# Performance work log

Measured on AMD Instinct MI355X. Metric: run time of the kernel, lower is better.

The kernel has to match this reference:

```python
import jax, jax.numpy as jnp
import numpy as np
import math

R, C, B, E = 64, 256, 1, 768
H, DK, F = 8, 96, 3072
EPS = 1e-5


def _ln(x, w, b):
    m = jnp.mean(x, axis=-1, keepdims=True)
    v = jnp.var(x, axis=-1, keepdims=True)
    return (x - m) / jnp.sqrt(v + EPS) * w + b


def _lin(x, w, b):
    # torch Linear: y = x @ W^T + b, W: [out, in]
    return jnp.einsum('...i,oi->...o', x, w) + b


def setup_inputs() -> dict:
    key = jax.random.key(0)
    ks = jax.random.split(key, 16)
    w = lambda k, s: jax.random.normal(k, s, dtype=jnp.float32) * 0.02
    z = lambda s: jnp.zeros(s, dtype=jnp.float32)
    o = lambda s: jnp.ones(s, dtype=jnp.float32)
    return {
        'x': jax.random.normal(ks[0], (R, C, B, E), dtype=jnp.float32),
        'ln_row_w': o((E,)), 'ln_row_b': z((E,)),
        'row_q_w': w(ks[1], (E, E)), 'row_q_b': z((E,)),
        'row_k_w': w(ks[2], (E, E)), 'row_k_b': z((E,)),
        'row_v_w': w(ks[3], (E, E)), 'row_v_b': z((E,)),
        'row_o_w': w(ks[4], (E, E)), 'row_o_b': z((E,)),
        'ln_col_w': o((E,)), 'ln_col_b': z((E,)),
        'col_q_w': w(ks[5], (E, E)), 'col_q_b': z((E,)),
        'col_k_w': w(ks[6], (E, E)), 'col_k_b': z((E,)),
        'col_v_w': w(ks[7], (E, E)), 'col_v_b': z((E,)),
        'col_o_w': w(ks[8], (E, E)), 'col_o_b': z((E,)),
        'ln_ffn_w': o((E,)), 'ln_ffn_b': z((E,)),
        'fc1_w': w(ks[9], (F, E)), 'fc1_b': z((F,)),
        'fc2_w': w(ks[10], (E, F)), 'fc2_b': z((E,)),
    }


def reference(x, ln_row_w, ln_row_b, row_q_w, row_q_b, row_k_w, row_k_b,
              row_v_w, row_v_b, row_o_w, row_o_b,
              ln_col_w, ln_col_b, col_q_w, col_q_b, col_k_w, col_k_b,
              col_v_w, col_v_b, col_o_w, col_o_b,
              ln_ffn_w, ln_ffn_b, fc1_w, fc1_b, fc2_w, fc2_b):
    r, c, n, e = x.shape  # n_rows, n_cols, batch, embed

    # ---- Row self-attention (pre-LN residual block) ----
    xn = _ln(x, ln_row_w, ln_row_b)
    scaling = (DK ** -0.5) / math.sqrt(r)  # align_scaling: extra 1/sqrt(n_rows)
    q = _lin(xn, row_q_w, row_q_b).reshape(r, c, n, H, DK) * scaling
    k = _lin(xn, row_k_w, row_k_b).reshape(r, c, n, H, DK)
    v = _lin(xn, row_v_w, row_v_b).reshape(r, c, n, H, DK)
    row_logits = jnp.einsum('rinhd,rjnhd->hnij', q, k)  # sums over rows
    row_probs = jax.nn.softmax(row_logits, axis=-1)     # [H, B, C, C]
    rc = jnp.einsum('hnij,rjnhd->rinhd', row_probs, v).reshape(r, c, n, e)
    x = x + _lin(rc, row_o_w, row_o_b)

    # ---- Column self-attention (pre-LN residual block) ----
    xn = _ln(x, ln_col_w, ln_col_b)
    q = _lin(xn, col_q_w, col_q_b).reshape(r, c, n, H, DK) * (DK ** -0.5)
    k = _lin(xn, col_k_w, col_k_b).reshape(r, c, n, H, DK)
    v = _lin(xn, col_v_w, col_v_b).reshape(r, c, n, H, DK)
    col_logits = jnp.einsum('icnhd,jcnhd->hcnij', q, k)
    col_probs = jax.nn.softmax(col_logits, axis=-1)     # [H, C, B, R, R]
    cc = jnp.einsum('hcnij,jcnhd->icnhd', col_probs, v).reshape(r, c, n, e)
    x = x + _lin(cc, col_o_w, col_o_b)

    # ---- Feed-forward (pre-LN residual block) ----
    xn = _ln(x, ln_ffn_w, ln_ffn_b)
    h = jax.nn.gelu(_lin(xn, fc1_w, fc1_b), approximate=False)
    x = x + _lin(h, fc2_w, fc2_b)

    return x, row_probs, col_probs
```

## Files before the change

kernel.cpp:

```cpp
#include <hip/hip_runtime.h>
#include <cstdint>

typedef unsigned short u16;
typedef __attribute__((ext_vector_type(8))) short short8;
typedef __attribute__((ext_vector_type(4))) short short4v;
typedef __attribute__((ext_vector_type(4))) float floatx4;

#define DEV __device__ __forceinline__

DEV float bf2f(u16 u) { union { uint32_t i; float f; } w; w.i = ((uint32_t)u) << 16; return w.f; }
DEV u16 f2bf(float f) {
  union { float f; uint32_t i; } w; w.f = f;
  uint32_t x = w.i;
  return (u16)((x + 0x7fffu + ((x >> 16) & 1u)) >> 16);
}

DEV float fast_gelu(float x) {
  const float y = x * 0.70710678118f;
  const float ay = fabsf(y);
  const float t = 1.f / (1.f + 0.3275911f * ay);
  const float poly = t * (0.254829592f + t * (-0.284496736f +
                     t * (1.421413741f + t * (-1.453152027f + t * 1.061405429f))));
  const float er = 1.f - poly * __expf(-y * y);
  const float erf_y = __builtin_copysignf(er, y);
  return 0.5f * x * (1.f + erf_y);
}

DEV void async_copy16(const u16* g, u16* l) {
  __builtin_amdgcn_global_load_lds(
      (const __attribute__((address_space(1))) void*)(uintptr_t)g,
      (__attribute__((address_space(3))) void*)(uint32_t)(uintptr_t)l,
      16, 0, 0);
}

struct CvtArgs {
  const float* src[10];
  float scale[10];
};
__global__ __launch_bounds__(256) void cvt_all(CvtArgs a, u16* __restrict__ dst) {
  const size_t e = ((size_t)blockIdx.x * 256 + threadIdx.x) * 4;
  if (e >= 9437184) return;
  int reg, N, K;
  size_t base;
  if (e < 4718592) { reg = (int)(e / 589824); base = (size_t)reg * 589824; N = 768; K = 768; }
  else if (e < 7077888) { reg = 8; base = 4718592; N = 3072; K = 768; }
  else { reg = 9; base = 7077888; N = 768; K = 3072; }
  const int NKT = K >> 5;
  const size_t r = e - base;
  const int tile = (int)(r >> 12);
  const int nt = tile / NKT, kt = tile - nt * NKT;
  const int rem = (int)(r & 4095);
  const int c = rem >> 10, row = (rem >> 3) & 127, j = rem & 7;
  const int n = nt * 128 + row, k = kt * 32 + c * 8 + j;
  const float sc = a.scale[reg];
  floatx4 f = *(const floatx4*)(a.src[reg] + (size_t)n * K + k);
  short4v o;
#pragma unroll
  for (int q = 0; q < 4; ++q) o[q] = (short)f2bf(f[q] * sc);
  *(short4v*)(dst + e) = o;
}

__global__ __launch_bounds__(256) void bias_pack(const float* __restrict__ qb,
                                                 const float* __restrict__ kb,
                                                 const float* __restrict__ vb,
                                                 float sq, float* __restrict__ out) {
  const int i = blockIdx.x * 256 + threadIdx.x;
  if (i >= 2304) return;
  const int buf = i / 768, c = i - buf * 768;
  out[i] = buf == 0 ? qb[c] * sq : (buf == 1 ? kb[c] : vb[c]);
}

template<bool INF32>
__global__ __launch_bounds__(256) void ln_kernel(const void* __restrict__ in,
                                                 const float* __restrict__ w,
                                                 const float* __restrict__ b,
                                                 u16* __restrict__ out) {
  const int wid = threadIdx.x >> 6, lane = threadIdx.x & 63;
  const int row = blockIdx.x * 4 + wid;
  const size_t base = (size_t)row * 768;
  float v[12];
#pragma unroll
  for (int p = 0; p < 3; ++p) {
    const int e = p * 256 + lane * 4;
    if constexpr (INF32) {
      floatx4 f = *(const floatx4*)((const float*)in + base + e);
#pragma unroll
      for (int j = 0; j < 4; ++j) v[p * 4 + j] = f[j];
    } else {
      short4v u = *(const short4v*)((const u16*)in + base + e);
#pragma unroll
      for (int j = 0; j < 4; ++j) v[p * 4 + j] = bf2f((u16)u[j]);
    }
  }
  float s = 0.f, sq = 0.f;
#pragma unroll
  for (int i = 0; i < 12; ++i) { s += v[i]; sq += v[i] * v[i]; }
#pragma unroll
  for (int m = 1; m < 64; m <<= 1) { s += __shfl_xor(s, m); sq += __shfl_xor(sq, m); }
  const float mean = s * (1.f / 768.f);
  const float var = sq * (1.f / 768.f) - mean * mean;
  const float rstd = rsqrtf(var + 1e-5f);
#pragma unroll
  for (int p = 0; p < 3; ++p) {
    const int e = p * 256 + lane * 4;
    floatx4 wv = *(const floatx4*)(w + e);
    floatx4 bv = *(const floatx4*)(b + e);
    short4v o;
#pragma unroll
    for (int j = 0; j < 4; ++j) {
      float y = (v[p * 4 + j] - mean) * rstd * wv[j] + bv[j];
      o[j] = (short)f2bf(y);
    }
    *(short4v*)(out + base + e) = o;
  }
}

template<int AMODE, int BP>
DEV void stage_tile(const u16* __restrict__ Ab, const u16* __restrict__ Bsrc,
                    int m0, int n0, int lda, int ldb, int kk0, int ktAbs, int t,
                    u16* ldsA, u16* ldsB) {
  const int wid = t >> 6, lane = t & 63;
  const int col = (((t & 3) ^ ((t >> 2) & 3)) << 3);
#pragma unroll
  for (int i = 0; i < 2; ++i) {
    const int r = i * 64 + (t >> 2);
    const int kk = kk0 + col;
    const u16* ga;
    if constexpr (AMODE == 0) {
      ga = Ab + (size_t)(m0 + r) * lda + kk;
    } else {
      const int r96 = kk / 96, d = kk - r96 * 96;
      ga = Ab + (size_t)r96 * 196608 + (size_t)(m0 + r) * 768 + d;
    }
    async_copy16(ga, ldsA + i * 2048 + wid * 512);

    const int slot = i * 4 + wid;
    if constexpr (BP) {
      const u16* gb = Bsrc + (size_t)ktAbs * 4096 + slot * 512 + lane * 8;
      async_copy16(gb, ldsB + slot * 512);
    } else {
      const u16* gb;
      if constexpr (AMODE == 0) {
        gb = Bsrc + (size_t)(n0 + r) * ldb + kk;
      } else {
        const int r96 = kk / 96, d = kk - r96 * 96;
        gb = Bsrc + (size_t)r96 * 196608 + (size_t)(n0 + r) * 768 + d;
      }
      async_copy16(gb, ldsB + i * 2048 + wid * 512);
    }
  }
}

template<int AMODE, int EPI, int BP>
__global__ __launch_bounds__(256) void gemm_bt(
    const u16* __restrict__ A, const u16* __restrict__ B,
    const float* __restrict__ bias, const void* __restrict__ res,
    void* __restrict__ out, int K, int lda, int ldb,
    long long aBatch, long long bBatch, long long outBatch, int ldc, int bkt0,
    float scale) {
  __shared__ u16 lds[3 * 8192];
  const int t = threadIdx.x;
  const int z = blockIdx.z;
  const int m0 = blockIdx.x * 128, n0 = blockIdx.y * 128;
  const u16* Ab;
  const u16* Bb;
  int koff = 0;
  if constexpr (AMODE == 0) { Ab = A + (size_t)z * aBatch; Bb = B + (size_t)z * bBatch; }
  else { const int h = z >> 4; Ab = A + h * 96; Bb = B + h * 96; koff = (z & 15) * 384; }

  const u16* Bstage;
  if constexpr (BP) Bstage = Bb + ((size_t)((n0 >> 7) * ldb + bkt0)) * 4096;
  else Bstage = Bb;

  const int wid = t >> 6, lane = t & 63;
  const int wr = wid >> 1, wc = wid & 1;
  const int lrow = lane & 15, lhi = lane >> 4;
  const int swl = lrow & 3;

  floatx4 acc[4][4];
#pragma unroll
  for (int i = 0; i < 4; ++i)
#pragma unroll
    for (int j = 0; j < 4; ++j) acc[i][j] = (floatx4){0.f, 0.f, 0.f, 0.f};

  const int NT = K >> 5;

  stage_tile<AMODE, BP>(Ab, Bstage, m0, n0, lda, ldb, koff, 0, t, lds, lds + 4096);
  if (NT > 1)
    stage_tile<AMODE, BP>(Ab, Bstage, m0, n0, lda, ldb, koff + 32, 1, t,
                          lds + 8192, lds + 8192 + 4096);
  if (NT > 2) asm volatile("s_waitcnt vmcnt(4)" ::: "memory");
  else        asm volatile("s_waitcnt vmcnt(0)" ::: "memory");
  __builtin_amdgcn_s_barrier();
  asm volatile("" ::: "memory");

  int cur = 0, nxt = 2;
  for (int kt = 0; kt < NT; ++kt) {
    const bool more = (kt + 2) < NT;
    if (more)
      stage_tile<AMODE, BP>(Ab, Bstage, m0, n0, lda, ldb, koff + (kt + 2) * 32, kt + 2, t,
                            lds + nxt * 8192, lds + nxt * 8192 + 4096);

    const u16* lA = lds + cur * 8192;
    const u16* lB = lA + 4096;
    short8 af[4], bfr[4];
#pragma unroll
    for (int mi = 0; mi < 4; ++mi)
      af[mi] = *(const short8*)&lA[(wr * 64 + mi * 16 + lrow) * 32 + ((lhi ^ swl) << 3)];
#pragma unroll
    for (int ni = 0; ni < 4; ++ni) {
      if constexpr (BP)
        bfr[ni] = *(const short8*)&lB[lhi * 1024 + (wc * 64 + ni * 16 + lrow) * 8];
      else
        bfr[ni] = *(const short8*)&lB[(wc * 64 + ni * 16 + lrow) * 32 + ((lhi ^ swl) << 3)];
    }

    __builtin_amdgcn_s_setprio(1);
#pragma unroll
    for (int mi = 0; mi < 4; ++mi)
#pragma unroll
      for (int ni = 0; ni < 4; ++ni)
        acc[mi][ni] = __builtin_amdgcn_mfma_f32_16x16x32_bf16(af[mi], bfr[ni], acc[mi][ni], 0, 0, 0);
    __builtin_amdgcn_s_setprio(0);

    if (kt + 1 < NT) {
      if (more) asm volatile("s_waitcnt vmcnt(4)" ::: "memory");
      else      asm volatile("s_waitcnt vmcnt(0)" ::: "memory");
      __builtin_amdgcn_s_barrier();
      asm volatile("" ::: "memory");
    }
    cur = (cur == 2) ? 0 : cur + 1;
    nxt = (nxt == 2) ? 0 : nxt + 1;
  }

  const int mbase = m0 + wr * 64;
  const int nbase = n0 + wc * 64;
#pragma unroll
  for (int mi = 0; mi < 4; ++mi) {
#pragma unroll
    for (int ni = 0; ni < 4; ++ni) {
      const int n = nbase + ni * 16 + lrow;
      float bz = 0.f;
      if constexpr (EPI != 1 && EPI != 7) { if (bias) bz = bias[n]; }
#pragma unroll
      for (int r4 = 0; r4 < 4; ++r4) {
        const int m = mbase + mi * 16 + lhi * 4 + r4;
        const float val = acc[mi][ni][r4];
        if constexpr (EPI == 1) {
          ((float*)out)[(size_t)z * outBatch + (size_t)m * ldc + n] = val;
        } else if constexpr (EPI == 2) {
          ((u16*)out)[(size_t)m * ldc + n] = f2bf(fast_gelu(val + bz));
        } else if constexpr (EPI == 3) {
          const float r = ((const float*)res)[(size_t)m * ldc + n];
          ((float*)out)[(size_t)m * ldc + n] = r + val + bz;
        } else if constexpr (EPI == 4) {
          const float r = ((const float*)res)[(size_t)m * ldc + n];
          ((u16*)out)[(size_t)m * ldc + n] = f2bf(r + val + bz);
        } else if constexpr (EPI == 5) {
          const float r = bf2f(((const u16*)res)[(size_t)m * ldc + n]);
          ((float*)out)[(size_t)m * ldc + n] = r + val + bz;
        } else if constexpr (EPI == 6) {
          const float r = bf2f(((const u16*)res)[(size_t)m * ldc + n]);
          ((u16*)out)[(size_t)m * ldc + n] = f2bf(r + val + bz);
        } else if constexpr (EPI == 7) {
          const int rr = n / 96, d = n - rr * 96;
          ((u16*)out)[((size_t)(rr * 256 + m)) * 768 + (size_t)z * 96 + d] = f2bf(val);
        } else if constexpr (EPI == 8) {
          const int buf = n / 768, col = n - buf * 768;
          ((u16*)out)[(size_t)buf * 12582912 + (size_t)m * 768 + col] = f2bf(val + bz);
        }
      }
    }
  }
}

__global__ __launch_bounds__(256) void softmax_row(const float* __restrict__ part,
                                                   float* __restrict__ probs_f,
                                                   u16* __restrict__ probs_b) {
  const int wid = threadIdx.x >> 6, lane = threadIdx.x & 63;
  const int row = blockIdx.x * 4 + wid;
  const int h = row >> 8, i = row & 255;
  const size_t base = (size_t)h * 16 * 65536 + (size_t)i * 256 + lane * 4;
  floatx4 v = (floatx4){0.f, 0.f, 0.f, 0.f};
#pragma unroll
  for (int s16 = 0; s16 < 16; ++s16) {
    floatx4 p = *(const floatx4*)(part + base + (size_t)s16 * 65536);
#pragma unroll
    for (int j = 0; j < 4; ++j) v[j] += p[j];
  }
  float mx = fmaxf(fmaxf(v[0], v[1]), fmaxf(v[2], v[3]));
#pragma unroll
  for (int m = 1; m < 64; m <<= 1) mx = fmaxf(mx, __shfl_xor(mx, m));
  float e[4], s = 0.f;
#pragma unroll
  for (int j = 0; j < 4; ++j) { e[j] = __expf(v[j] - mx); s += e[j]; }
#pragma unroll
  for (int m = 1; m < 64; m <<= 1) s += __shfl_xor(s, m);
  const float inv = 1.f / s;
  floatx4 of;
  short4v ob;
#pragma unroll
  for (int j = 0; j < 4; ++j) {
    const float p = e[j] * inv;
    of[j] = p;
    ob[j] = (short)f2bf(p);
  }
  *(floatx4*)(probs_f + (size_t)row * 256 + lane * 4) = of;
  *(short4v*)(probs_b + (size_t)row * 256 + lane * 4) = ob;
}

__global__ __launch_bounds__(256) void pack_vt(const u16* __restrict__ v, u16* __restrict__ vt) {
  __shared__ u16 S[64][104];
  const int jb = blockIdx.x, r = blockIdx.y, h = blockIdx.z;
  const int t = threadIdx.x;
#pragma unroll
  for (int p = 0; p < 3; ++p) {
    const int cid = t + p * 256;
    const int j = cid / 12, ch = cid - j * 12;
    short8 x = *(const short8*)&v[((size_t)(r * 256 + jb * 64 + j)) * 768 + h * 96 + ch * 8];
    *(short8*)&S[j][ch * 8] = x;
  }
  __syncthreads();
#pragma unroll
  for (int p = 0; p < 3; ++p) {
    const int cid = t + p * 256;
    const int d = cid / 8, cj = cid - d * 8;
    u16 tmp[8];
#pragma unroll
    for (int m = 0; m < 8; ++m) tmp[m] = S[cj * 8 + m][d];
    const int row_t = r * 96 + d;
    const int k = jb * 64 + cj * 8;
    const size_t off = (size_t)h * 1572864 +
                       ((size_t)((row_t >> 7) * 8 + (k >> 5))) * 4096 +
                       ((k >> 3) & 3) * 1024 + (row_t & 127) * 8;
    *(short8*)&vt[off] = *(short8*)tmp;
  }
}

__global__ __launch_bounds__(256) void col_attn(const u16* __restrict__ q,
                                                const u16* __restrict__ k,
                                                const u16* __restrict__ v,
                                                float* __restrict__ probs,
                                                u16* __restrict__ ctx) {
  __shared__ u16 qs[64][104];
  __shared__ u16 ks[64][104];
  __shared__ u16 vt[96][72];
  __shared__ u16 ps[64][72];
  const int c = blockIdx.x, h = blockIdx.y;
  const int t = threadIdx.x;
#pragma unroll
  for (int p = 0; p < 3; ++p) {
    const int cid = t + p * 256;
    const int i = cid / 12, ch = cid - i * 12;
    const size_t g = ((size_t)(i * 256 + c)) * 768 + h * 96 + ch * 8;
    short8 qv = *(const short8*)(q + g);
    short8 kv = *(const short8*)(k + g);
    short8 vv = *(const short8*)(v + g);
    *(short8*)&qs[i][ch * 8] = qv;
    *(short8*)&ks[i][ch * 8] = kv;
#pragma unroll
    for (int m = 0; m < 8; ++m) vt[ch * 8 + m][i] = (u16)vv[m];
  }
  __syncthreads();
  const int lane = t & 63, wid = t >> 6;
  const int lrow = lane & 15, lhi = lane >> 4;

  floatx4 s[4];
#pragma unroll
  for (int nj = 0; nj < 4; ++nj) s[nj] = (floatx4){0.f, 0.f, 0.f, 0.f};
#pragma unroll
  for (int kk = 0; kk < 3; ++kk) {
    short8 a = *(const short8*)&qs[wid * 16 + lrow][kk * 32 + lhi * 8];
#pragma unroll
    for (int nj = 0; nj < 4; ++nj) {
      short8 bb = *(const short8*)&ks[nj * 16 + lrow][kk * 32 + lhi * 8];
      s[nj] = __builtin_amdgcn_mfma_f32_16x16x32_bf16(a, bb, s[nj], 0, 0, 0);
    }
  }
  const size_t pb = ((size_t)(h * 256 + c)) * 4096;
#pragma unroll
  for (int r4 = 0; r4 < 4; ++r4) {
    float mx = fmaxf(fmaxf(s[0][r4], s[1][r4]), fmaxf(s[2][r4], s[3][r4]));
    mx = fmaxf(mx, __shfl_xor(mx, 1));
    mx = fmaxf(mx, __shfl_xor(mx, 2));
    mx = fmaxf(mx, __shfl_xor(mx, 4));
    mx = fmaxf(mx, __shfl_xor(mx, 8));
    float e[4], sum = 0.f;
#pragma unroll
    for (int nj = 0; nj < 4; ++nj) { e[nj] = __expf(s[nj][r4] - mx); sum += e[nj]; }
    sum += __shfl_xor(sum, 1);
    sum += __shfl_xor(sum, 2);
    sum += __shfl_xor(sum, 4);
    sum += __shfl_xor(sum, 8);
    const float inv = 1.f / sum;
    const int i = wid * 16 + lhi * 4 + r4;
#pragma unroll
    for (int nj = 0; nj < 4; ++nj) {
      const float pv = e[nj] * inv;
      const int j = nj * 16 + lrow;
      probs[pb + (size_t)i * 64 + j] = pv;
      ps[i][j] = f2bf(pv);
    }
  }
  __syncthreads();
  floatx4 o[6];
#pragma unroll
  for (int df = 0; df < 6; ++df) o[df] = (floatx4){0.f, 0.f, 0.f, 0.f};
#pragma unroll
  for (int k2 = 0; k2 < 2; ++k2) {
    short8 a = *(const short8*)&ps[wid * 16 + lrow][k2 * 32 + lhi * 8];
#pragma unroll
    for (int df = 0; df < 6; ++df) {
      short8 bb = *(const short8*)&vt[df * 16 + lrow][k2 * 32 + lhi * 8];
      o[df] = __builtin_amdgcn_mfma_f32_16x16x32_bf16(a, bb, o[df], 0, 0, 0);
    }
  }
#pragma unroll
  for (int df = 0; df < 6; ++df)
#pragma unroll
    for (int r4 = 0; r4 < 4; ++r4) {
      const int i = wid * 16 + lhi * 4 + r4;
      const int d = df * 16 + lrow;
      ctx[((size_t)(i * 256 + c)) * 768 + h * 96 + d] = f2bf(o[df][r4]);
    }
}

extern "C" void kernel_launch(void* const* d_in, const int* in_sizes, int n_in,
                              void* d_out, int out_size, void* d_ws, size_t ws_size,
                              hipStream_t stream) {
  const float* x_in  = (const float*)d_in[0];
  const float* lnr_w = (const float*)d_in[1];
  const float* lnr_b = (const float*)d_in[2];
  const float* rq_w  = (const float*)d_in[3];
  const float* rq_b  = (const float*)d_in[4];
  const float* rk_w  = (const float*)d_in[5];
  const float* rk_b  = (const float*)d_in[6];
  const float* rv_w  = (const float*)d_in[7];
  const float* rv_b  = (const float*)d_in[8];
  const float* ro_w  = (const float*)d_in[9];
  const float* ro_b  = (const float*)d_in[10];
  const float* lnc_w = (const float*)d_in[11];
  const float* lnc_b = (const float*)d_in[12];
  const float* cq_w  = (const float*)d_in[13];
  const float* cq_b  = (const float*)d_in[14];
  const float* ck_w  = (const float*)d_in[15];
  const float* ck_b  = (const float*)d_in[16];
  const float* cv_w  = (const float*)d_in[17];
  const float* cv_b  = (const float*)d_in[18];
  const float* co_w  = (const float*)d_in[19];
  const float* co_b  = (const float*)d_in[20];
  const float* lnf_w = (const float*)d_in[21];
  const float* lnf_b = (const float*)d_in[22];
  const float* f1_w  = (const float*)d_in[23];
  const float* f1_b  = (const float*)d_in[24];
  const float* f2_w  = (const float*)d_in[25];
  const float* f2_b  = (const float*)d_in[26];

  const float s_row = 0.0127577591f;
  const float s_col = 0.1020620726f;

  char* ws = (char*)d_ws;
  const size_t WSZ_E = 589824 * 2;
  u16* w_all = (u16*)ws;
  u16* w_rqkv = w_all;
  u16* w_ro   = (u16*)(ws + 3 * WSZ_E);
  u16* w_cqkv = (u16*)(ws + 4 * WSZ_E);
  u16* w_co   = (u16*)(ws + 7 * WSZ_E);
  u16* w_f1   = (u16*)(ws + 8 * WSZ_E);
  u16* w_f2   = (u16*)(ws + 8 * WSZ_E + 4718592);
  size_t off = 8 * WSZ_E + 2 * 4718592;

  const bool xf32 = ws_size >= 147849216ULL;
  char* x_cur = ws + off;
  off += xf32 ? 50331648 : 25165824;
  u16* qb = (u16*)(ws + off); off += 25165824;
  u16* kb = (u16*)(ws + off); off += 25165824;
  u16* vb = (u16*)(ws + off); off += 25165824;
  u16* probsb = (u16*)(ws + off); off += 1048576;
  float* qkvb_row = (float*)(ws + off); off += 9216;
  float* qkvb_col = (float*)(ws + off); off += 9216;

  u16* vt     = qb;
  u16* ctx1   = kb;
  u16* hidden = qb;
  u16* xn3    = vb;

  float* out_x  = (float*)d_out;
  float* out_rp = out_x + 12582912;
  float* out_cp = out_x + 13107200;
  u16* xn   = (u16*)out_x;
  u16* ctx2 = (u16*)((char*)out_x + 25165824);
  float* part = out_x;

  const dim3 blk(256);

  CvtArgs ca;
  ca.src[0] = rq_w; ca.src[1] = rk_w; ca.src[2] = rv_w; ca.src[3] = ro_w;
  ca.src[4] = cq_w; ca.src[5] = ck_w; ca.src[6] = cv_w; ca.src[7] = co_w;
  ca.src[8] = f1_w; ca.src[9] = f2_w;
  for (int i = 0; i < 10; ++i) ca.scale[i] = 1.f;
  ca.scale[0] = s_row; ca.scale[4] = s_col;
  cvt_all<<<9216, blk, 0, stream>>>(ca, w_all);
  bias_pack<<<9, blk, 0, stream>>>(rq_b, rk_b, rv_b, s_row, qkvb_row);
  bias_pack<<<9, blk, 0, stream>>>(cq_b, ck_b, cv_b, s_col, qkvb_col);

  ln_kernel<true><<<4096, blk, 0, stream>>>(x_in, lnr_w, lnr_b, xn);
  gemm_bt<0, 8, 1><<<dim3(128, 18, 1), blk, 0, stream>>>(xn, w_rqkv, qkvb_row, nullptr, qb, 768, 768, 24, 0, 0, 0, 768, 0, 1.f);
  gemm_bt<2, 1, 0><<<dim3(2, 2, 128), blk, 0, stream>>>(qb, kb, nullptr, nullptr, part, 384, 0, 0, 0, 0, 65536LL, 256, 0, 1.f);
  softmax_row<<<512, blk, 0, stream>>>(part, out_rp, probsb);
  pack_vt<<<dim3(4, 64, 8), blk, 0, stream>>>(vb, vt);
  gemm_bt<0, 7, 1><<<dim3(2, 48, 8), blk, 0, stream>>>(probsb, vt, nullptr, nullptr, ctx1, 256, 256, 8, 65536LL, 1572864LL, 0, 0, 0, 1.f);
  if (xf32)
    gemm_bt<0, 3, 1><<<dim3(128, 6, 1), blk, 0, stream>>>(ctx1, w_ro, ro_b, x_in, x_cur, 768, 768, 24, 0, 0, 0, 768, 0, 1.f);
  else
    gemm_bt<0, 4, 1><<<dim3(128, 6, 1), blk, 0, stream>>>(ctx1, w_ro, ro_b, x_in, x_cur, 768, 768, 24, 0, 0, 0, 768, 0, 1.f);

  if (xf32) ln_kernel<true><<<4096, blk, 0, stream>>>(x_cur, lnc_w, lnc_b, xn);
  else      ln_kernel<false><<<4096, blk, 0, stream>>>(x_cur, lnc_w, lnc_b, xn);
  gemm_bt<0, 8, 1><<<dim3(128, 18, 1), blk, 0, stream>>>(xn, w_cqkv, qkvb_col, nullptr, qb, 768, 768, 24, 0, 0, 0, 768, 0, 1.f);
  col_attn<<<dim3(256, 8), blk, 0, stream>>>(qb, kb, vb, out_cp, ctx2);
  if (xf32)
    gemm_bt<0, 3, 1><<<dim3(128, 6, 1), blk, 0, stream>>>(ctx2, w_co, co_b, x_cur, x_cur, 768, 768, 24, 0, 0, 0, 768, 0, 1.f);
  else
    gemm_bt<0, 6, 1><<<dim3(128, 6, 1), blk, 0, stream>>>(ctx2, w_co, co_b, x_cur, x_cur, 768, 768, 24, 0, 0, 0, 768, 0, 1.f);

  if (xf32) ln_kernel<true><<<4096, blk, 0, stream>>>(x_cur, lnf_w, lnf_b, xn3);
  else      ln_kernel<false><<<4096, blk, 0, stream>>>(x_cur, lnf_w, lnf_b, xn3);
  gemm_bt<0, 2, 1><<<dim3(128, 12, 1), blk, 0, stream>>>(xn3, w_f1, f1_b, nullptr, hidden, 768, 768, 24, 0, 0, 0, 1536, 0, 1.f);
  if (xf32)
    gemm_bt<0, 3, 1><<<dim3(128, 6, 1), blk, 0, stream>>>(hidden, w_f2, f2_b, x_cur, out_x, 1536, 1536, 96, 0, 0, 0, 768, 0, 1.f);
  else
    gemm_bt<0, 5, 1><<<dim3(128, 6, 1), blk, 0, stream>>>(hidden, w_f2, f2_b, x_cur, out_x, 1536, 1536, 96, 0, 0, 0, 768, 0, 1.f);
  gemm_bt<0, 2, 1><<<dim3(128, 12, 1), blk, 0, stream>>>(xn3, w_f1 + 1536 * 768, f1_b + 1536, nullptr, hidden, 768, 768, 24, 0, 0, 0, 1536, 0, 1.f);
  gemm_bt<0, 3, 1><<<dim3(128, 6, 1), blk, 0, stream>>>(hidden, w_f2, nullptr, out_x, out_x, 1536, 1536, 96, 0, 0, 0, 768, 48, 1.f);
}
```

Before: 618.9 us.

## Pre-pack GEMM A operands into tiled layout in producer kernels

The LayerNorm, softmax, column-attention, P·V and GELU kernels now write their bf16 outputs directly in the 128x32 k-tile packed layout that the B weights already use. The GEMM gains an AP template path that stages A with contiguous async copies and reads LDS fragments without the XOR swizzle. The aim is to cut address arithmetic and scattered global reads in the GEMM mainloop. The cost is more scattered stores in producer epilogues. The bf16-residual variants (EPI 5/6) are dropped, so the non-f32 path now reads the residual as float.

```diff
diff --git a/kernel.cpp b/kernel.cpp
--- a/kernel.cpp
+++ b/kernel.cpp
@@ -13,6 +13,11 @@
   union { float f; uint32_t i; } w; w.f = f;
   uint32_t x = w.i;
   return (u16)((x + 0x7fffu + ((x >> 16) & 1u)) >> 16);
+}
+
+DEV size_t poff(int row, int k, int nkt) {
+  return ((size_t)((row >> 7) * nkt + (k >> 5))) * 4096 +
+         (size_t)(((k >> 3) & 3) * 1024 + (row & 127) * 8 + (k & 7));
 }
 
 DEV float fast_gelu(float x) {
@@ -111,33 +116,35 @@
       float y = (v[p * 4 + j] - mean) * rstd * wv[j] + bv[j];
       o[j] = (short)f2bf(y);
     }
-    *(short4v*)(out + base + e) = o;
-  }
-}
-
-template<int AMODE, int BP>
-DEV void stage_tile(const u16* __restrict__ Ab, const u16* __restrict__ Bsrc,
+    *(short4v*)(out + poff(row, e, 24)) = o;
+  }
+}
+
+template<int AMODE, int AP, int BP>
+DEV void stage_tile(const u16* __restrict__ Asrc, const u16* __restrict__ Bsrc,
                     int m0, int n0, int lda, int ldb, int kk0, int ktAbs, int t,
                     u16* ldsA, u16* ldsB) {
   const int wid = t >> 6, lane = t & 63;
   const int col = (((t & 3) ^ ((t >> 2) & 3)) << 3);
 #pragma unroll
   for (int i = 0; i < 2; ++i) {
+    const int slot = i * 4 + wid;
     const int r = i * 64 + (t >> 2);
     const int kk = kk0 + col;
-    const u16* ga;
-    if constexpr (AMODE == 0) {
-      ga = Ab + (size_t)(m0 + r) * lda + kk;
+    if constexpr (AP) {
+      async_copy16(Asrc + (size_t)ktAbs * 4096 + slot * 512 + lane * 8, ldsA + slot * 512);
     } else {
-      const int r96 = kk / 96, d = kk - r96 * 96;
-      ga = Ab + (size_t)r96 * 196608 + (size_t)(m0 + r) * 768 + d;
-    }
-    async_copy16(ga, ldsA + i * 2048 + wid * 512);
-
-    const int slot = i * 4 + wid;
+      const u16* ga;
+      if constexpr (AMODE == 0) {
+        ga = Asrc + (size_t)(m0 + r) * lda + kk;
+      } else {
+        const int r96 = kk / 96, d = kk - r96 * 96;
+        ga = Asrc + (size_t)r96 * 196608 + (size_t)(m0 + r) * 768 + d;
+      }
+      async_copy16(ga, ldsA + i * 2048 + wid * 512);
+    }
     if constexpr (BP) {
-      const u16* gb = Bsrc + (size_t)ktAbs * 4096 + slot * 512 + lane * 8;
-      async_copy16(gb, ldsB + slot * 512);
+      async_copy16(Bsrc + (size_t)ktAbs * 4096 + slot * 512 + lane * 8, ldsB + slot * 512);
     } else {
       const u16* gb;
       if constexpr (AMODE == 0) {
@@ -151,7 +158,7 @@
   }
 }
 
-template<int AMODE, int EPI, int BP>
+template<int AMODE, int EPI, int AP, int BP>
 __global__ __launch_bounds__(256) void gemm_bt(
     const u16* __restrict__ A, const u16* __restrict__ B,
     const float* __restrict__ bias, const void* __restrict__ res,
@@ -168,7 +175,10 @@
   if constexpr (AMODE == 0) { Ab = A + (size_t)z * aBatch; Bb = B + (size_t)z * bBatch; }
   else { const int h = z >> 4; Ab = A + h * 96; Bb = B + h * 96; koff = (z & 15) * 384; }
 
+  const u16* Astage;
   const u16* Bstage;
+  if constexpr (AP) Astage = Ab + ((size_t)((m0 >> 7) * lda)) * 4096;
+  else Astage = Ab;
   if constexpr (BP) Bstage = Bb + ((size_t)((n0 >> 7) * ldb + bkt0)) * 4096;
   else Bstage = Bb;
 
@@ -185,10 +195,10 @@
 
   const int NT = K >> 5;
 
-  stage_tile<AMODE, BP>(Ab, Bstage, m0, n0, lda, ldb, koff, 0, t, lds, lds + 4096);
+  stage_tile<AMODE, AP, BP>(Astage, Bstage, m0, n0, lda, ldb, koff, 0, t, lds, lds + 4096);
   if (NT > 1)
-    stage_tile<AMODE, BP>(Ab, Bstage, m0, n0, lda, ldb, koff + 32, 1, t,
-                          lds + 8192, lds + 8192 + 4096);
+    stage_tile<AMODE, AP, BP>(Astage, Bstage, m0, n0, lda, ldb, koff + 32, 1, t,
+                              lds + 8192, lds + 8192 + 4096);
   if (NT > 2) asm volatile("s_waitcnt vmcnt(4)" ::: "memory");
   else        asm volatile("s_waitcnt vmcnt(0)" ::: "memory");
   __builtin_amdgcn_s_barrier();
@@ -198,15 +208,19 @@
   for (int kt = 0; kt < NT; ++kt) {
     const bool more = (kt + 2) < NT;
     if (more)
-      stage_tile<AMODE, BP>(Ab, Bstage, m0, n0, lda, ldb, koff + (kt + 2) * 32, kt + 2, t,
-                            lds + nxt * 8192, lds + nxt * 8192 + 4096);
+      stage_tile<AMODE, AP, BP>(Astage, Bstage, m0, n0, lda, ldb, koff + (kt + 2) * 32,
+                                kt + 2, t, lds + nxt * 8192, lds + nxt * 8192 + 4096);
 
     const u16* lA = lds + cur * 8192;
     const u16* lB = lA + 4096;
     short8 af[4], bfr[4];
 #pragma unroll
-    for (int mi = 0; mi < 4; ++mi)
-      af[mi] = *(const short8*)&lA[(wr * 64 + mi * 16 + lrow) * 32 + ((lhi ^ swl) << 3)];
+    for (int mi = 0; mi < 4; ++mi) {
+      if constexpr (AP)
+        af[mi] = *(const short8*)&lA[lhi * 1024 + (wr * 64 + mi * 16 + lrow) * 8];
+      else
+        af[mi] = *(const short8*)&lA[(wr * 64 + mi * 16 + lrow) * 32 + ((lhi ^ swl) << 3)];
+    }
 #pragma unroll
     for (int ni = 0; ni < 4; ++ni) {
       if constexpr (BP)
@@ -249,22 +263,16 @@
         if constexpr (EPI == 1) {
           ((float*)out)[(size_t)z * outBatch + (size_t)m * ldc + n] = val;
         } else if constexpr (EPI == 2) {
-          ((u16*)out)[(size_t)m * ldc + n] = f2bf(fast_gelu(val + bz));
+          ((u16*)out)[poff(m, n, ldc >> 5)] = f2bf(fast_gelu(val + bz));
         } else if constexpr (EPI == 3) {
           const float r = ((const float*)res)[(size_t)m * ldc + n];
           ((float*)out)[(size_t)m * ldc + n] = r + val + bz;
         } else if constexpr (EPI == 4) {
           const float r = ((const float*)res)[(size_t)m * ldc + n];
           ((u16*)out)[(size_t)m * ldc + n] = f2bf(r + val + bz);
-        } else if constexpr (EPI == 5) {
-          const float r = bf2f(((const u16*)res)[(size_t)m * ldc + n]);
-          ((float*)out)[(size_t)m * ldc + n] = r + val + bz;
-        } else if constexpr (EPI == 6) {
-          const float r = bf2f(((const u16*)res)[(size_t)m * ldc + n]);
-          ((u16*)out)[(size_t)m * ldc + n] = f2bf(r + val + bz);
         } else if constexpr (EPI == 7) {
           const int rr = n / 96, d = n - rr * 96;
-          ((u16*)out)[((size_t)(rr * 256 + m)) * 768 + (size_t)z * 96 + d] = f2bf(val);
+          ((u16*)out)[poff(rr * 256 + m, z * 96 + d, 24)] = f2bf(val);
         } else if constexpr (EPI == 8) {
           const int buf = n / 768, col = n - buf * 768;
           ((u16*)out)[(size_t)buf * 12582912 + (size_t)m * 768 + col] = f2bf(val + bz);
@@ -306,7 +314,7 @@
     ob[j] = (short)f2bf(p);
   }
   *(floatx4*)(probs_f + (size_t)row * 256 + lane * 4) = of;
-  *(short4v*)(probs_b + (size_t)row * 256 + lane * 4) = ob;
+  *(short4v*)(probs_b + (size_t)h * 65536 + poff(i, lane * 4, 8)) = ob;
 }
 
 __global__ __launch_bounds__(256) void pack_vt(const u16* __restrict__ v, u16* __restrict__ vt) {
@@ -330,10 +338,7 @@
     for (int m = 0; m < 8; ++m) tmp[m] = S[cj * 8 + m][d];
     const int row_t = r * 96 + d;
     const int k = jb * 64 + cj * 8;
-    const size_t off = (size_t)h * 1572864 +
-                       ((size_t)((row_t >> 7) * 8 + (k >> 5))) * 4096 +
-                       ((k >> 3) & 3) * 1024 + (row_t & 127) * 8;
-    *(short8*)&vt[off] = *(short8*)tmp;
+    *(short8*)&vt[(size_t)h * 1572864 + poff(row_t, k, 8)] = *(short8*)tmp;
   }
 }
 
@@ -421,7 +426,7 @@
     for (int r4 = 0; r4 < 4; ++r4) {
       const int i = wid * 16 + lhi * 4 + r4;
       const int d = df * 16 + lrow;
-      ctx[((size_t)(i * 256 + c)) * 768 + h * 96 + d] = f2bf(o[df][r4]);
+      ctx[poff(i * 256 + c, h * 96 + d, 24)] = f2bf(o[df][r4]);
     }
 }
 
@@ -505,32 +510,29 @@
   bias_pack<<<9, blk, 0, stream>>>(cq_b, ck_b, cv_b, s_col, qkvb_col);
 
   ln_kernel<true><<<4096, blk, 0, stream>>>(x_in, lnr_w, lnr_b, xn);
-  gemm_bt<0, 8, 1><<<dim3(128, 18, 1), blk, 0, stream>>>(xn, w_rqkv, qkvb_row, nullptr, qb, 768, 768, 24, 0, 0, 0, 768, 0, 1.f);
-  gemm_bt<2, 1, 0><<<dim3(2, 2, 128), blk, 0, stream>>>(qb, kb, nullptr, nullptr, part, 384, 0, 0, 0, 0, 65536LL, 256, 0, 1.f);
+  gemm_bt<0, 8, 1, 1><<<dim3(128, 18, 1), blk, 0, stream>>>(xn, w_rqkv, qkvb_row, nullptr, qb, 768, 24, 24, 0, 0, 0, 768, 0, 1.f);
+  gemm_bt<2, 1, 0, 0><<<dim3(2, 2, 128), blk, 0, stream>>>(qb, kb, nullptr, nullptr, part, 384, 0, 0, 0, 0, 65536LL, 256, 0, 1.f);
   softmax_row<<<512, blk, 0, stream>>>(part, out_rp, probsb);
   pack_vt<<<dim3(4, 64, 8), blk, 0, stream>>>(vb, vt);
-  gemm_bt<0, 7, 1><<<dim3(2, 48, 8), blk, 0, stream>>>(probsb, vt, nullptr, nullptr, ctx1, 256, 256, 8, 65536LL, 1572864LL, 0, 0, 0, 1.f);
+  gemm_bt<0, 7, 1, 1><<<dim3(2, 48, 8), blk, 0, stream>>>(probsb, vt, nullptr, nullptr, ctx1, 256, 8, 8, 65536LL, 1572864LL, 0, 0, 0, 1.f);
   if (xf32)
-    gemm_bt<0, 3, 1><<<dim3(128, 6, 1), blk, 0, stream>>>(ctx1, w_ro, ro_b, x_in, x_cur, 768, 768, 24, 0, 0, 0, 768, 0, 1.f);
+    gemm_bt<0, 3, 1, 1><<<dim3(128, 6, 1), blk, 0, stream>>>(ctx1, w_ro, ro_b, x_in, x_cur, 768, 24, 24, 0, 0, 0, 768, 0, 1.f);
   else
-    gemm_bt<0, 4, 1><<<dim3(128, 6, 1), blk, 0, stream>>>(ctx1, w_ro, ro_b, x_in, x_cur, 768, 768, 24, 0, 0, 0, 768, 0, 1.f);
+    gemm_bt<0, 4, 1, 1><<<dim3(128, 6, 1), blk, 0, stream>>>(ctx1, w_ro, ro_b, x_in, x_cur, 768, 24, 24, 0, 0, 0, 768, 0, 1.f);
 
   if (xf32) ln_kernel<true><<<4096, blk, 0, stream>>>(x_cur, lnc_w, lnc_b, xn);
   else      ln_kernel<false><<<4096, blk, 0, stream>>>(x_cur, lnc_w, lnc_b, xn);
-  gemm_bt<0, 8, 1><<<dim3(128, 18, 1), blk, 0, stream>>>(xn, w_cqkv, qkvb_col, nullptr, qb, 768, 768, 24, 0, 0, 0, 768, 0, 1.f);
+  gemm_bt<0, 8, 1, 1><<<dim3(128, 18, 1), blk, 0, stream>>>(xn, w_cqkv, qkvb_col, nullptr, qb, 768, 24, 24, 0, 0, 0, 768, 0, 1.f);
   col_attn<<<dim3(256, 8), blk, 0, stream>>>(qb, kb, vb, out_cp, ctx2);
   if (xf32)
-    gemm_bt<0, 3, 1><<<dim3(128, 6, 1), blk, 0, stream>>>(ctx2, w_co, co_b, x_cur, x_cur, 768, 768, 24, 0, 0, 0, 768, 0, 1.f);
+    gemm_bt<0, 3, 1, 1><<<dim3(128, 6, 1), blk, 0, stream>>>(ctx2, w_co, co_b, x_cur, x_cur, 768, 24, 24, 0, 0, 0, 768, 0, 1.f);
   else
-    gemm_bt<0, 6, 1><<<dim3(128, 6, 1), blk, 0, stream>>>(ctx2, w_co, co_b, x_cur, x_cur, 768, 768, 24, 0, 0, 0, 768, 0, 1.f);
+    gemm_bt<0, 4, 1, 1><<<dim3(128, 6, 1), blk, 0, stream>>>(ctx2, w_co, co_b, x_cur, x_cur, 768, 24, 24, 0, 0, 0, 768, 0, 1.f);
 
   if (xf32) ln_kernel<true><<<4096, blk, 0, stream>>>(x_cur, lnf_w, lnf_b, xn3);
   else      ln_kernel<false><<<4096, blk, 0, stream>>>(x_cur, lnf_w, lnf_b, xn3);
-  gemm_bt<0, 2, 1><<<dim3(128, 12, 1), blk, 0, stream>>>(xn3, w_f1, f1_b, nullptr, hidden, 768, 768, 24, 0, 0, 0, 1536, 0, 1.f);
-  if (xf32)
-    gemm_bt<0, 3, 1><<<dim3(128, 6, 1), blk, 0, stream>>>(hidden, w_f2, f2_b, x_cur, out_x, 1536, 1536, 96, 0, 0, 0, 768, 0, 1.f);
-  else
-    gemm_bt<0, 5, 1><<<dim3(128, 6, 1), blk, 0, stream>>>(hidden, w_f2, f2_b, x_cur, out_x, 1536, 1536, 96, 0, 0, 0, 768, 0, 1.f);
-  gemm_bt<0, 2, 1><<<dim3(128, 12, 1), blk, 0, stream>>>(xn3, w_f1 + 1536 * 768, f1_b + 1536, nullptr, hidden, 768, 768, 24, 0, 0, 0, 1536, 0, 1.f);
-  gemm_bt<0, 3, 1><<<dim3(128, 6, 1), blk, 0, stream>>>(hidden, w_f2, nullptr, out_x, out_x, 1536, 1536, 96, 0, 0, 0, 768, 48, 1.f);
-}
+  gemm_bt<0, 2, 1, 1><<<dim3(128, 12, 1), blk, 0, stream>>>(xn3, w_f1, f1_b, nullptr, hidden, 768, 24, 24, 0, 0, 0, 1536, 0, 1.f);
+  gemm_bt<0, 3, 1, 1><<<dim3(128, 6, 1), blk, 0, stream>>>(hidden, w_f2, f2_b, x_cur, out_x, 1536, 48, 96, 0, 0, 0, 768, 0, 1.f);
+  gemm_bt<0, 2, 1, 1><<<dim3(128, 12, 1), blk, 0, stream>>>(xn3, w_f1 + 1536 * 768, f1_b + 1536, nullptr, hidden, 768, 24, 24, 0, 0, 0, 1536, 0, 1.f);
+  gemm_bt<0, 3, 1, 1><<<dim3(128, 6, 1), blk, 0, stream>>>(hidden, w_f2, nullptr, out_x, out_x, 1536, 48, 96, 0, 0, 0, 768, 48, 1.f);
+}
```

Result: no change. 624.2 us (+0.8%).
